# Kernel tuning notes

Measured on AMD Instinct MI355X. Metric: run time of the kernel, lower is better.

## Reference

```python
import jax, jax.numpy as jnp
import numpy as np
from jax import lax

T = 16          # timesteps
EPS = 1e-12     # torch F.normalize eps
DN = ('NCHW', 'OIHW', 'NCHW')

def conv2d(x, w, pad):
    return lax.conv_general_dilated(x, w, (1, 1), [(pad, pad), (pad, pad)],
                                    dimension_numbers=DN)

def setup_inputs() -> dict:
    key = jax.random.key(0)
    ks = jax.random.split(key, 7)
    B, C, H, W, K = 16, 512, 14, 14, 64
    return {
        'input_tensor': jax.random.normal(ks[0], (B * T, C, H, W), jnp.float32),
        'centers': jax.random.normal(ks[1], (K, C), jnp.float32) * 0.05,
        'share_w': jax.random.normal(ks[2], (K, C, 1, 1), jnp.float32) * 0.05,
        'share_b': jax.random.uniform(ks[3], (K,), jnp.float32),
        'U_z': jax.random.normal(ks[4], (K, K, 3, 3), jnp.float32) * 0.05,
        'U_r': jax.random.normal(ks[5], (K, K, 3, 3), jnp.float32) * 0.05,
        'U_h': jax.random.normal(ks[6], (K, K, 3, 3), jnp.float32) * 0.05,
    }

def reference(input_tensor, centers, share_w, share_b, U_z, U_r, U_h):
    NT, C, H, W = input_tensor.shape
    B = NT // T
    K = centers.shape[0]

    # soft-assignment pre-activation: 1x1 conv (SAME) -> [B*T, K, H, W]
    wxb = conv2d(input_tensor, share_w, 0) + share_b[None, :, None, None]
    wxb = wxb.reshape(B, T, K, H, W).transpose(1, 0, 2, 3, 4)  # [T,B,K,H,W]

    def gru_step(h, wxb_t):
        z = jax.nn.sigmoid(wxb_t + conv2d(h, U_z, 1))
        r = jax.nn.sigmoid(wxb_t + conv2d(h, U_r, 1))
        hh = jnp.tanh(wxb_t + conv2d(r * h, U_h, 1))
        h_new = (1.0 - z) * hh + z * h
        return h_new, h_new

    h0 = jnp.zeros((B, K, H, W), input_tensor.dtype)
    _, assign = lax.scan(gru_step, h0, wxb)            # [T,B,K,H,W]
    assign = assign.transpose(1, 0, 2, 3, 4).reshape(B * T, K, H * W)

    a_sum = assign.sum(-1, keepdims=True)              # [BT,K,1]
    a = a_sum * centers[None]                          # [BT,K,C]
    feats = input_tensor.reshape(B * T, C, H * W)
    x = jnp.einsum('nks,ncs->nkc', assign, feats)      # [BT,K,C]

    vlad = (x - a).reshape(B, T, K, C).sum(1)          # [B,K,C]
    vlad = vlad / jnp.maximum(jnp.linalg.norm(vlad, axis=2, keepdims=True), EPS)
    vlad = vlad.reshape(B, K * C)
    vlad = vlad / jnp.maximum(jnp.linalg.norm(vlad, axis=1, keepdims=True), EPS)
    return vlad
```

## Files before the change

kernel.cpp:

```cpp
#include <hip/hip_runtime.h>

#define Bc 16
#define Tc 16
#define Cc 512
#define Kc 64
#define Sc 196
#define KS (Kc*Sc)
#define BKS (Bc*Kc*Sc)
#define TBKS (Tc*BKS)
#define GFIN (16*64*512)
#define PART_N (8*GFIN)
#define PX 256
#define PLB2 (Kc*PX)
#define NUTT 110592

typedef __attribute__((ext_vector_type(8))) short bf16x8;
typedef __attribute__((ext_vector_type(4))) float f32x4;

__device__ __forceinline__ float sigmoid_f(float x) { return 1.f / (1.f + __expf(-x)); }
__device__ __forceinline__ float tanh_f(float x) { return 1.f - 2.f / (__expf(2.f * x) + 1.f); }

__device__ __forceinline__ float b2f(unsigned short u) {
    return __uint_as_float(((unsigned)u) << 16);
}
__device__ __forceinline__ unsigned short f2b(float f) {
    unsigned u = __float_as_uint(f);
    return (unsigned short)((u + 0x7FFFu + ((u >> 16) & 1u)) >> 16);
}
__device__ __forceinline__ void split1(float f, unsigned short& h, unsigned short& l) {
    unsigned u = __float_as_uint(f);
    unsigned uh = u & 0xffff0000u;
    h = (unsigned short)(uh >> 16);
    float fl = f - __uint_as_float(uh);
    l = (unsigned short)(__float_as_uint(fl) >> 16);
}

__global__ __launch_bounds__(256) void k_transpose_w(const float* __restrict__ w, float* __restrict__ wt) {
    int idx = blockIdx.x * 256 + threadIdx.x;
    if (idx < Kc * Cc) {
        int k = idx & 63, c = idx >> 6;
        wt[idx] = w[k * Cc + c];
    }
}

__global__ __launch_bounds__(256) void k_prep_u(const float* __restrict__ Uz,
        const float* __restrict__ Ur, const float* __restrict__ Uh,
        unsigned short* __restrict__ uth, unsigned short* __restrict__ utl) {
    int idx = blockIdx.x * 256 + threadIdx.x;
    int ki = idx & 63;
    int ko = (idx >> 6) & 63;
    int gt = idx >> 12;
    int tap = gt % 9, g = gt / 9;
    const float* U = (g == 0) ? Uz : (g == 1) ? Ur : Uh;
    float v = U[((size_t)ko * 64 + ki) * 9 + tap];
    unsigned short h, l;
    split1(v, h, l);
    uth[idx] = h; utl[idx] = l;
}

__global__ __launch_bounds__(256) void k_init(float4* __restrict__ h32,
        float4* __restrict__ h16, float4* __restrict__ rh16) {
    const int i = blockIdx.x * 256 + threadIdx.x;
    const float4 z = make_float4(0.f, 0.f, 0.f, 0.f);
    h32[i] = z;
    if (i < 32768) { h16[i] = z; rh16[i] = z; }
}

__global__ __launch_bounds__(256) void k_conv1x1(const float* __restrict__ x, const float* __restrict__ wt,
        const float* __restrict__ bias, float* __restrict__ wxb,
        float* __restrict__ assign0, float* __restrict__ hplane32,
        unsigned short* __restrict__ hplane16) {
    __shared__ float Xs[64][64];
    const int tid = threadIdx.x;
    const int gs0 = blockIdx.x * 64;
    const int kw = __builtin_amdgcn_readfirstlane((tid >> 6) << 4);
    const int lane = tid & 63;
    const int rbase = (tid >> 6) * 16;
    const int gs_c = gs0 + lane;
    const int n_c = gs_c / Sc, s_c = gs_c - n_c * Sc;
    const float* xcol = x + (size_t)n_c * (Cc * Sc) + s_c;

    float xr[16];
#pragma unroll
    for (int q = 0; q < 16; ++q) xr[q] = xcol[(size_t)(rbase + q) * Sc];
    float acc[16] = {};
    for (int c0 = 0; c0 < Cc; c0 += 64) {
        __syncthreads();
#pragma unroll
        for (int q = 0; q < 16; ++q) Xs[rbase + q][lane] = xr[q];
        __syncthreads();
        if (c0 + 64 < Cc) {
#pragma unroll
            for (int q = 0; q < 16; ++q) xr[q] = xcol[(size_t)(c0 + 64 + rbase + q) * Sc];
        }
#pragma unroll 8
        for (int cc = 0; cc < 64; ++cc) {
            const float xv = Xs[cc][lane];
            const float* wp = wt + (size_t)(c0 + cc) * Kc + kw;
#pragma unroll
            for (int i = 0; i < 16; ++i) acc[i] += wp[i] * xv;
        }
    }
    const int t = n_c & 15, bb = n_c >> 4;
    float* op = wxb + (((size_t)t * Bc + bb) * Kc + kw) * Sc + s_c;
    const int px0 = (s_c / 14 + 1) * 16 + (s_c - (s_c / 14) * 14 + 1);
#pragma unroll
    for (int i = 0; i < 16; ++i) {
        float v = acc[i] + bias[kw + i];
        op[(size_t)i * Sc] = v;
        if (t == 0) {
            float a = (1.f - sigmoid_f(v)) * tanh_f(v);
            assign0[((size_t)bb * Kc + kw + i) * Sc + s_c] = a;
            const size_t pp = (size_t)bb * PLB2 + (size_t)px0 * 64 + kw + i;
            hplane32[pp] = a; hplane16[pp] = f2b(a);
        }
    }
}

__global__ __launch_bounds__(128) void k_gru_gates(const unsigned short* __restrict__ hplane16,
        const float* __restrict__ wxb_t, const unsigned short* __restrict__ uth,
        const unsigned short* __restrict__ utl,
        float* __restrict__ zb, unsigned short* __restrict__ rhplane16) {
    const int b = blockIdx.x, yrow = blockIdx.y + 1, gate = blockIdx.z;
    const int pxb = yrow * 16;
    const int tid = threadIdx.x;
    const int nh = tid >> 6;
    const int lane = tid & 63;
    const int lg = lane >> 4, ln = lane & 15;
    const unsigned short* hp = hplane16 + (size_t)b * PLB2;
    const unsigned short* ug_h = uth + (size_t)gate * 36864;
    const unsigned short* ug_l = utl + (size_t)gate * 36864;

    f32x4 acc[2];
    acc[0] = (f32x4){0.f, 0.f, 0.f, 0.f};
    acc[1] = (f32x4){0.f, 0.f, 0.f, 0.f};
#pragma unroll
    for (int tap = 0; tap < 9; ++tap) {
        const int toff = (tap / 3 - 1) * 16 + (tap % 3 - 1);
        int arow = pxb + ln + toff;
        arow = min(max(arow, 0), 255);
        const unsigned short* abase = hp + (size_t)arow * 64;
#pragma unroll
        for (int ks = 0; ks < 2; ++ks) {
            bf16x8 A = *(const bf16x8*)(abase + ks * 32 + lg * 8);
#pragma unroll
            for (int nt = 0; nt < 2; ++nt) {
                const int ko_t = (nh * 2 + nt) * 16;
                const size_t bo = ((size_t)tap * 64 + ko_t + ln) * 64 + ks * 32 + lg * 8;
                bf16x8 Bh = *(const bf16x8*)(ug_h + bo);
                bf16x8 Bl = *(const bf16x8*)(ug_l + bo);
                acc[nt] = __builtin_amdgcn_mfma_f32_16x16x32_bf16(A, Bh, acc[nt], 0, 0, 0);
                acc[nt] = __builtin_amdgcn_mfma_f32_16x16x32_bf16(A, Bl, acc[nt], 0, 0, 0);
            }
        }
    }
#pragma unroll
    for (int nt = 0; nt < 2; ++nt) {
        const int ko = (nh * 2 + nt) * 16 + ln;
#pragma unroll
        for (int r = 0; r < 4; ++r) {
            const int i = lg * 4 + r;
            if (i >= 1 && i <= 14) {
                const int s = (yrow - 1) * 14 + (i - 1);
                const size_t cs = ((size_t)b * Kc + ko) * Sc + s;
                float sv = sigmoid_f(wxb_t[cs] + acc[nt][r]);
                if (gate == 0) {
                    zb[cs] = sv;
                } else {
                    const int px = pxb + i;
                    float hv = b2f(hp[(size_t)px * 64 + ko]);
                    rhplane16[(size_t)b * PLB2 + (size_t)px * 64 + ko] = f2b(sv * hv);
                }
            }
        }
    }
}

__global__ __launch_bounds__(256) void k_gru_out(const unsigned short* __restrict__ rhplane16,
        const float* __restrict__ wxb_t, const unsigned short* __restrict__ uth,
        const unsigned short* __restrict__ utl, const float* __restrict__ zb,
        float* __restrict__ hplane32, unsigned short* __restrict__ hplane16,
        float* __restrict__ assign_t) {
    const int b = blockIdx.x, yrow = blockIdx.y + 1;
    const int pxb = yrow * 16;
    const int tid = threadIdx.x;
    const int nt = tid >> 6;
    const int lane = tid & 63;
    const int lg = lane >> 4, ln = lane & 15;
    const unsigned short* rp = rhplane16 + (size_t)b * PLB2;
    const unsigned short* uh0 = uth + (size_t)2 * 36864;
    const unsigned short* ul0 = utl + (size_t)2 * 36864;

    f32x4 acc = (f32x4){0.f, 0.f, 0.f, 0.f};
#pragma unroll
    for (int tap = 0; tap < 9; ++tap) {
        const int toff = (tap / 3 - 1) * 16 + (tap % 3 - 1);
        int arow = pxb + ln + toff;
        arow = min(max(arow, 0), 255);
        const unsigned short* abase = rp + (size_t)arow * 64;
#pragma unroll
        for (int ks = 0; ks < 2; ++ks) {
            bf16x8 A = *(const bf16x8*)(abase + ks * 32 + lg * 8);
            const size_t bo = ((size_t)tap * 64 + nt * 16 + ln) * 64 + ks * 32 + lg * 8;
            bf16x8 Bh = *(const bf16x8*)(uh0 + bo);
            bf16x8 Bl = *(const bf16x8*)(ul0 + bo);
            acc = __builtin_amdgcn_mfma_f32_16x16x32_bf16(A, Bh, acc, 0, 0, 0);
            acc = __builtin_amdgcn_mfma_f32_16x16x32_bf16(A, Bl, acc, 0, 0, 0);
        }
    }
    const int ko = nt * 16 + ln;
#pragma unroll
    for (int r = 0; r < 4; ++r) {
        const int i = lg * 4 + r;
        if (i >= 1 && i <= 14) {
            const int s = (yrow - 1) * 14 + (i - 1);
            const size_t cs = ((size_t)b * Kc + ko) * Sc + s;
            const int px = pxb + i;
            const size_t pp = (size_t)b * PLB2 + (size_t)px * 64 + ko;
            float pre = wxb_t[cs];
            float zv = zb[cs];
            float hpv = hplane32[pp];
            float hh = tanh_f(pre + acc[r]);
            float hn = (1.f - zv) * hh + zv * hpv;
            hplane32[pp] = hn;
            hplane16[pp] = f2b(hn);
            assign_t[cs] = hn;
        }
    }
}

__global__ __launch_bounds__(512) void k_einsum(const float* __restrict__ x, const float* __restrict__ assign,
                                                float* __restrict__ part) {
    extern __shared__ float lds[];
    unsigned short* Ah = (unsigned short*)lds;
    unsigned short* Al = Ah + 64 * 40;
    unsigned short* Xh = Al + 64 * 40;
    unsigned short* Xl = Xh + 128 * 40;
    const int cq = blockIdx.x, tg = blockIdx.y, b = blockIdx.z;
    const int tid = threadIdx.x;
    const int wv = tid >> 6, lane = tid & 63;
    const int lg = lane >> 4, ln = lane & 15;
    const int ka = tid >> 3, ss4 = (tid & 7) * 4;
    const int cx = tid >> 2, ss8 = (tid & 3) * 8;

    f32x4 acc[4];
#pragma unroll
    for (int mt = 0; mt < 4; ++mt) acc[mt] = (f32x4){0.f, 0.f, 0.f, 0.f};

    for (int tt = 0; tt < 2; ++tt) {
        const int t = tg * 2 + tt;
        const int n = b * Tc + t;
        const float* ap = assign + ((size_t)t * Bc + b) * KS;
        const float* xp = x + ((size_t)n * Cc + cq * 128) * Sc;
        for (int sc7 = 0; sc7 < 7; ++sc7) {
            const int s0 = sc7 * 32;
            __syncthreads();
            {
                float4 v = make_float4(0.f, 0.f, 0.f, 0.f);
                if (s0 + ss4 <= 192) v = *(const float4*)(ap + (size_t)ka * Sc + s0 + ss4);
                ushort4 h, l;
                split1(v.x, h.x, l.x); split1(v.y, h.y, l.y);
                split1(v.z, h.z, l.z); split1(v.w, h.w, l.w);
                *(ushort4*)(Ah + ka * 40 + ss4) = h;
                *(ushort4*)(Al + ka * 40 + ss4) = l;
            }
#pragma unroll
            for (int q = 0; q < 2; ++q) {
                const int so = ss8 + q * 4;
                float4 v = make_float4(0.f, 0.f, 0.f, 0.f);
                if (s0 + so <= 192) v = *(const float4*)(xp + (size_t)cx * Sc + s0 + so);
                ushort4 h, l;
                split1(v.x, h.x, l.x); split1(v.y, h.y, l.y);
                split1(v.z, h.z, l.z); split1(v.w, h.w, l.w);
                *(ushort4*)(Xh + cx * 40 + so) = h;
                *(ushort4*)(Xl + cx * 40 + so) = l;
            }
            __syncthreads();
            bf16x8 Bh = *(const bf16x8*)(Xh + (wv * 16 + ln) * 40 + lg * 8);
            bf16x8 Bl = *(const bf16x8*)(Xl + (wv * 16 + ln) * 40 + lg * 8);
#pragma unroll
            for (int mt = 0; mt < 4; ++mt) {
                bf16x8 Af = *(const bf16x8*)(Ah + (mt * 16 + ln) * 40 + lg * 8);
                bf16x8 Alo = *(const bf16x8*)(Al + (mt * 16 + ln) * 40 + lg * 8);
                acc[mt] = __builtin_amdgcn_mfma_f32_16x16x32_bf16(Af, Bh, acc[mt], 0, 0, 0);
                acc[mt] = __builtin_amdgcn_mfma_f32_16x16x32_bf16(Alo, Bh, acc[mt], 0, 0, 0);
                acc[mt] = __builtin_amdgcn_mfma_f32_16x16x32_bf16(Af, Bl, acc[mt], 0, 0, 0);
            }
        }
    }
    const int c = cq * 128 + wv * 16 + ln;
#pragma unroll
    for (int mt = 0; mt < 4; ++mt) {
#pragma unroll
        for (int r = 0; r < 4; ++r) {
            const int k = mt * 16 + lg * 4 + r;
            part[(((size_t)tg * Bc + b) * Kc + k) * Cc + c] = acc[mt][r];
        }
    }
}

__global__ __launch_bounds__(256) void k_reduce(const float* __restrict__ assign, const float* __restrict__ part,
        const float* __restrict__ centers, float* __restrict__ vlad, float* __restrict__ norm2) {
    __shared__ float redw[4];
    __shared__ float a_s;
    const int blk = blockIdx.x;
    const int b = blk >> 6, k = blk & 63;
    const int tid = threadIdx.x;
    const int wave = tid >> 6, lane = tid & 63;
    const size_t bkoff = ((size_t)b * Kc + k) * Sc;
    float s = 0.f;
    for (int q = tid; q < 784; q += 256) {
        int t = q / 49, s4 = q - t * 49;
        float4 v = *(const float4*)(assign + (size_t)t * BKS + bkoff + s4 * 4);
        s += (v.x + v.y) + (v.z + v.w);
    }
#pragma unroll
    for (int o = 1; o < 64; o <<= 1) s += __shfl_xor(s, o);
    if (lane == 0) redw[wave] = s;
    __syncthreads();
    if (tid == 0) a_s = redw[0] + redw[1] + redw[2] + redw[3];
    __syncthreads();
    const float a = a_s;
    const size_t base = ((size_t)b * Kc + k) * Cc;
    const int c = tid * 2;
    float2 acc2 = make_float2(0.f, 0.f);
#pragma unroll
    for (int g = 0; g < 8; ++g) {
        float2 p = *(const float2*)(part + (size_t)g * GFIN + base + c);
        acc2.x += p.x; acc2.y += p.y;
    }
    float2 cv = *(const float2*)(centers + (size_t)k * Cc + c);
    float v0 = acc2.x - a * cv.x, v1 = acc2.y - a * cv.y;
    *(float2*)(vlad + base + c) = make_float2(v0, v1);
    float ss = v0 * v0 + v1 * v1;
#pragma unroll
    for (int o = 1; o < 64; o <<= 1) ss += __shfl_xor(ss, o);
    __syncthreads();
    if (lane == 0) redw[wave] = ss;
    __syncthreads();
    if (tid == 0) norm2[blk] = redw[0] + redw[1] + redw[2] + redw[3];
}

__global__ __launch_bounds__(64) void k_norms(const float* __restrict__ norm2, float* __restrict__ scl) {
    const int b = blockIdx.x;
    const int k = threadIdx.x;
    float ss = norm2[b * Kc + k];
    float inv = 1.f / fmaxf(sqrtf(ss), 1e-12f);
    float g = ss * inv * inv;
#pragma unroll
    for (int o = 1; o < 64; o <<= 1) g += __shfl_xor(g, o);
    float gi = 1.f / fmaxf(sqrtf(g), 1e-12f);
    scl[b * Kc + k] = inv * gi;
}

__global__ __launch_bounds__(256) void k_scale(const float* __restrict__ vlad, const float* __restrict__ scl,
                                               float* __restrict__ out) {
    const int blk = blockIdx.x;
    const int b = blk >> 4, kt = blk & 15;
    const int tid = threadIdx.x;
    const int kk = tid >> 6, lane = tid & 63;
    const int k = kt * 4 + kk;
    const float sv = scl[b * Kc + k];
    const float* vp = vlad + ((size_t)b * Kc + k) * Cc + lane * 8;
    float* op = out + ((size_t)b * Kc + k) * Cc + lane * 8;
    float4 v0 = *(const float4*)vp;
    float4 v1 = *(const float4*)(vp + 4);
    *(float4*)op = make_float4(v0.x * sv, v0.y * sv, v0.z * sv, v0.w * sv);
    *(float4*)(op + 4) = make_float4(v1.x * sv, v1.y * sv, v1.z * sv, v1.w * sv);
}

extern "C" void kernel_launch(void* const* d_in, const int* in_sizes, int n_in,
                              void* d_out, int out_size, void* d_ws, size_t ws_size,
                              hipStream_t stream) {
    (void)in_sizes; (void)n_in; (void)out_size; (void)ws_size;
    const float* x       = (const float*)d_in[0];
    const float* centers = (const float*)d_in[1];
    const float* share_w = (const float*)d_in[2];
    const float* share_b = (const float*)d_in[3];
    const float* Uz      = (const float*)d_in[4];
    const float* Ur      = (const float*)d_in[5];
    const float* Uh      = (const float*)d_in[6];
    float* out = (float*)d_out;
    float* ws  = (float*)d_ws;

    float* part      = ws;
    float* vlad      = ws;
    float* wxb       = ws;
    unsigned short* rhplane16 = (unsigned short*)(ws + (size_t)TBKS);
    unsigned short* hplane16  = (unsigned short*)(ws + (size_t)TBKS + 131072);
    float* assign   = ws + (size_t)PART_N;
    float* zb       = assign + (size_t)TBKS;
    float* hplane32 = zb + (size_t)BKS;
    float* wt       = hplane32 + (size_t)Bc * PLB2;
    unsigned short* utt_h = (unsigned short*)(wt + 32768);
    unsigned short* utt_l = utt_h + NUTT;
    float* norm2    = wt + 32768 + NUTT;
    float* scl      = norm2 + (size_t)Bc * Kc;

    const size_t ein_lds = (64 * 40 + 128 * 40) * 2 * 2;

    k_transpose_w<<<dim3(128), 256, 0, stream>>>(share_w, wt);
    k_prep_u<<<dim3(432), 256, 0, stream>>>(Uz, Ur, Uh, utt_h, utt_l);
    k_init<<<dim3(256), 256, 0, stream>>>((float4*)hplane32, (float4*)hplane16, (float4*)rhplane16);
    k_conv1x1<<<dim3(784), 256, 0, stream>>>(x, wt, share_b, wxb, assign, hplane32, hplane16);
    for (int t = 1; t < Tc; ++t) {
        k_gru_gates<<<dim3(16, 14, 2), 128, 0, stream>>>(hplane16, wxb + (size_t)t * BKS,
                                                         utt_h, utt_l, zb, rhplane16);
        k_gru_out<<<dim3(16, 14), 256, 0, stream>>>(rhplane16, wxb + (size_t)t * BKS,
                                                    utt_h, utt_l, zb, hplane32, hplane16,
                                                    assign + (size_t)t * BKS);
    }
    k_einsum<<<dim3(4, 8, 16), 512, ein_lds, stream>>>(x, assign, part);
    k_reduce<<<dim3(Bc * Kc), 256, 0, stream>>>(assign, part, centers, vlad, norm2);
    k_norms<<<dim3(Bc), 64, 0, stream>>>(norm2, scl);
    k_scale<<<dim3(256), 256, 0, stream>>>(vlad, scl, out);
}
```

Measured before the change: 455.7 us.

## Fuse GRU gate and output kernels into one step kernel with LDS r*h halo

Merges the two per-timestep GRU kernels into a single kernel. Three waves recompute the r gate for the centre row and its neighbour rows into a swizzled LDS tile, one wave computes z into LDS, and two waves then run the U_h convolution from LDS. The bf16 hidden plane is double-buffered across timesteps to avoid read/write races, which halves the launch count in the 15-step loop and removes the global round trips for z and r*h. In exchange, the r gate is computed redundantly for halo rows, and only two of the four waves run the final convolution.

```diff
diff --git a/kernel.cpp b/kernel.cpp
--- a/kernel.cpp
+++ b/kernel.cpp
@@ -58,12 +58,11 @@
     uth[idx] = h; utl[idx] = l;
 }
 
-__global__ __launch_bounds__(256) void k_init(float4* __restrict__ h32,
-        float4* __restrict__ h16, float4* __restrict__ rh16) {
+__global__ __launch_bounds__(256) void k_init(float4* __restrict__ h32, float4* __restrict__ h16) {
     const int i = blockIdx.x * 256 + threadIdx.x;
     const float4 z = make_float4(0.f, 0.f, 0.f, 0.f);
     h32[i] = z;
-    if (i < 32768) { h16[i] = z; rh16[i] = z; }
+    h16[i] = z;
 }
 
 __global__ __launch_bounds__(256) void k_conv1x1(const float* __restrict__ x, const float* __restrict__ wt,
@@ -117,114 +116,116 @@
     }
 }
 
-__global__ __launch_bounds__(128) void k_gru_gates(const unsigned short* __restrict__ hplane16,
-        const float* __restrict__ wxb_t, const unsigned short* __restrict__ uth,
-        const unsigned short* __restrict__ utl,
-        float* __restrict__ zb, unsigned short* __restrict__ rhplane16) {
-    const int b = blockIdx.x, yrow = blockIdx.y + 1, gate = blockIdx.z;
-    const int pxb = yrow * 16;
+__global__ __launch_bounds__(256) void k_gru_step(const unsigned short* __restrict__ h16r,
+        unsigned short* __restrict__ h16w, float* __restrict__ hplane32,
+        const float* __restrict__ wxb_t,
+        const unsigned short* __restrict__ uth, const unsigned short* __restrict__ utl,
+        float* __restrict__ assign_t) {
+    __shared__ unsigned short rhS[48 * 64];
+    __shared__ float zS[16 * 68];
+    const int b = blockIdx.x, y0 = blockIdx.y + 1;
     const int tid = threadIdx.x;
-    const int nh = tid >> 6;
-    const int lane = tid & 63;
+    const int w = tid >> 6, lane = tid & 63;
     const int lg = lane >> 4, ln = lane & 15;
-    const unsigned short* hp = hplane16 + (size_t)b * PLB2;
-    const unsigned short* ug_h = uth + (size_t)gate * 36864;
-    const unsigned short* ug_l = utl + (size_t)gate * 36864;
-
-    f32x4 acc[2];
-    acc[0] = (f32x4){0.f, 0.f, 0.f, 0.f};
-    acc[1] = (f32x4){0.f, 0.f, 0.f, 0.f};
-#pragma unroll
-    for (int tap = 0; tap < 9; ++tap) {
-        const int toff = (tap / 3 - 1) * 16 + (tap % 3 - 1);
-        int arow = pxb + ln + toff;
-        arow = min(max(arow, 0), 255);
-        const unsigned short* abase = hp + (size_t)arow * 64;
-#pragma unroll
-        for (int ks = 0; ks < 2; ++ks) {
-            bf16x8 A = *(const bf16x8*)(abase + ks * 32 + lg * 8);
-#pragma unroll
-            for (int nt = 0; nt < 2; ++nt) {
-                const int ko_t = (nh * 2 + nt) * 16;
-                const size_t bo = ((size_t)tap * 64 + ko_t + ln) * 64 + ks * 32 + lg * 8;
-                bf16x8 Bh = *(const bf16x8*)(ug_h + bo);
-                bf16x8 Bl = *(const bf16x8*)(ug_l + bo);
-                acc[nt] = __builtin_amdgcn_mfma_f32_16x16x32_bf16(A, Bh, acc[nt], 0, 0, 0);
-                acc[nt] = __builtin_amdgcn_mfma_f32_16x16x32_bf16(A, Bl, acc[nt], 0, 0, 0);
-            }
-        }
-    }
-#pragma unroll
-    for (int nt = 0; nt < 2; ++nt) {
-        const int ko = (nh * 2 + nt) * 16 + ln;
-#pragma unroll
-        for (int r = 0; r < 4; ++r) {
-            const int i = lg * 4 + r;
-            if (i >= 1 && i <= 14) {
-                const int s = (yrow - 1) * 14 + (i - 1);
-                const size_t cs = ((size_t)b * Kc + ko) * Sc + s;
-                float sv = sigmoid_f(wxb_t[cs] + acc[nt][r]);
-                if (gate == 0) {
-                    zb[cs] = sv;
+    const unsigned short* hp = h16r + (size_t)b * PLB2;
+
+    {
+        const int prow = (w < 3) ? (y0 - 1 + w) : y0;
+        const int gsel = (w < 3) ? 1 : 0;
+        const unsigned short* gh = uth + (size_t)gsel * 36864;
+        const unsigned short* gl = utl + (size_t)gsel * 36864;
+        f32x4 acc[4];
+#pragma unroll
+        for (int nt = 0; nt < 4; ++nt) acc[nt] = (f32x4){0.f, 0.f, 0.f, 0.f};
+#pragma unroll
+        for (int tap = 0; tap < 9; ++tap) {
+            const int toff = (tap / 3 - 1) * 16 + (tap % 3 - 1);
+            int arow = prow * 16 + ln + toff;
+            arow = min(max(arow, 0), 255);
+            const unsigned short* ab = hp + (size_t)arow * 64;
+#pragma unroll
+            for (int ks = 0; ks < 2; ++ks) {
+                bf16x8 A = *(const bf16x8*)(ab + ks * 32 + lg * 8);
+#pragma unroll
+                for (int nt = 0; nt < 4; ++nt) {
+                    const size_t bo = ((size_t)tap * 64 + nt * 16 + ln) * 64 + ks * 32 + lg * 8;
+                    bf16x8 Bh = *(const bf16x8*)(gh + bo);
+                    bf16x8 Bl = *(const bf16x8*)(gl + bo);
+                    acc[nt] = __builtin_amdgcn_mfma_f32_16x16x32_bf16(A, Bh, acc[nt], 0, 0, 0);
+                    acc[nt] = __builtin_amdgcn_mfma_f32_16x16x32_bf16(A, Bl, acc[nt], 0, 0, 0);
+                }
+            }
+        }
+        const int srow = prow - 1;
+#pragma unroll
+        for (int nt = 0; nt < 4; ++nt) {
+#pragma unroll
+            for (int r = 0; r < 4; ++r) {
+                const int i = lg * 4 + r;
+                const int ko = nt * 16 + ln;
+                const bool sval = (srow >= 0 && srow < 14 && i >= 1 && i <= 14);
+                const int s = sval ? srow * 14 + (i - 1) : 0;
+                const float pre = wxb_t[((size_t)b * Kc + ko) * Sc + s];
+                const float g = sigmoid_f(pre + acc[nt][r]);
+                if (w < 3) {
+                    const int px = prow * 16 + i;
+                    const float hv = b2f(hp[(size_t)px * 64 + ko]);
+                    const int lpx = w * 16 + i;
+                    *(unsigned short*)((char*)rhS + lpx * 128 + ((ko << 1) ^ ((lpx & 7) << 4))) = f2b(g * hv);
                 } else {
-                    const int px = pxb + i;
-                    float hv = b2f(hp[(size_t)px * 64 + ko]);
-                    rhplane16[(size_t)b * PLB2 + (size_t)px * 64 + ko] = f2b(sv * hv);
+                    zS[i * 68 + ko] = g;
                 }
             }
         }
     }
-}
-
-__global__ __launch_bounds__(256) void k_gru_out(const unsigned short* __restrict__ rhplane16,
-        const float* __restrict__ wxb_t, const unsigned short* __restrict__ uth,
-        const unsigned short* __restrict__ utl, const float* __restrict__ zb,
-        float* __restrict__ hplane32, unsigned short* __restrict__ hplane16,
-        float* __restrict__ assign_t) {
-    const int b = blockIdx.x, yrow = blockIdx.y + 1;
-    const int pxb = yrow * 16;
-    const int tid = threadIdx.x;
-    const int nt = tid >> 6;
-    const int lane = tid & 63;
-    const int lg = lane >> 4, ln = lane & 15;
-    const unsigned short* rp = rhplane16 + (size_t)b * PLB2;
-    const unsigned short* uh0 = uth + (size_t)2 * 36864;
-    const unsigned short* ul0 = utl + (size_t)2 * 36864;
-
-    f32x4 acc = (f32x4){0.f, 0.f, 0.f, 0.f};
-#pragma unroll
-    for (int tap = 0; tap < 9; ++tap) {
-        const int toff = (tap / 3 - 1) * 16 + (tap % 3 - 1);
-        int arow = pxb + ln + toff;
-        arow = min(max(arow, 0), 255);
-        const unsigned short* abase = rp + (size_t)arow * 64;
-#pragma unroll
-        for (int ks = 0; ks < 2; ++ks) {
-            bf16x8 A = *(const bf16x8*)(abase + ks * 32 + lg * 8);
-            const size_t bo = ((size_t)tap * 64 + nt * 16 + ln) * 64 + ks * 32 + lg * 8;
-            bf16x8 Bh = *(const bf16x8*)(uh0 + bo);
-            bf16x8 Bl = *(const bf16x8*)(ul0 + bo);
-            acc = __builtin_amdgcn_mfma_f32_16x16x32_bf16(A, Bh, acc, 0, 0, 0);
-            acc = __builtin_amdgcn_mfma_f32_16x16x32_bf16(A, Bl, acc, 0, 0, 0);
-        }
-    }
-    const int ko = nt * 16 + ln;
-#pragma unroll
-    for (int r = 0; r < 4; ++r) {
-        const int i = lg * 4 + r;
-        if (i >= 1 && i <= 14) {
-            const int s = (yrow - 1) * 14 + (i - 1);
-            const size_t cs = ((size_t)b * Kc + ko) * Sc + s;
-            const int px = pxb + i;
-            const size_t pp = (size_t)b * PLB2 + (size_t)px * 64 + ko;
-            float pre = wxb_t[cs];
-            float zv = zb[cs];
-            float hpv = hplane32[pp];
-            float hh = tanh_f(pre + acc[r]);
-            float hn = (1.f - zv) * hh + zv * hpv;
-            hplane32[pp] = hn;
-            hplane16[pp] = f2b(hn);
-            assign_t[cs] = hn;
+    __syncthreads();
+    if (w < 2) {
+        const unsigned short* hh_t = uth + (size_t)2 * 36864;
+        const unsigned short* hl_t = utl + (size_t)2 * 36864;
+        f32x4 a2[2];
+        a2[0] = (f32x4){0.f, 0.f, 0.f, 0.f};
+        a2[1] = (f32x4){0.f, 0.f, 0.f, 0.f};
+#pragma unroll
+        for (int tap = 0; tap < 9; ++tap) {
+            const int toff = (tap / 3 - 1) * 16 + (tap % 3 - 1);
+            int la = 16 + ln + toff;
+            la = min(max(la, 0), 47);
+#pragma unroll
+            for (int ks = 0; ks < 2; ++ks) {
+                bf16x8 A = *(const bf16x8*)((const char*)rhS + la * 128 +
+                                            (((ks * 64 + lg * 16)) ^ ((la & 7) << 4)));
+#pragma unroll
+                for (int nt2 = 0; nt2 < 2; ++nt2) {
+                    const int kot = (w * 2 + nt2) * 16;
+                    const size_t bo = ((size_t)tap * 64 + kot + ln) * 64 + ks * 32 + lg * 8;
+                    bf16x8 Bh = *(const bf16x8*)(hh_t + bo);
+                    bf16x8 Bl = *(const bf16x8*)(hl_t + bo);
+                    a2[nt2] = __builtin_amdgcn_mfma_f32_16x16x32_bf16(A, Bh, a2[nt2], 0, 0, 0);
+                    a2[nt2] = __builtin_amdgcn_mfma_f32_16x16x32_bf16(A, Bl, a2[nt2], 0, 0, 0);
+                }
+            }
+        }
+#pragma unroll
+        for (int nt2 = 0; nt2 < 2; ++nt2) {
+#pragma unroll
+            for (int r = 0; r < 4; ++r) {
+                const int i = lg * 4 + r;
+                if (i >= 1 && i <= 14) {
+                    const int ko = (w * 2 + nt2) * 16 + ln;
+                    const int s = (y0 - 1) * 14 + (i - 1);
+                    const size_t cs = ((size_t)b * Kc + ko) * Sc + s;
+                    const int px = y0 * 16 + i;
+                    const size_t pp = (size_t)b * PLB2 + (size_t)px * 64 + ko;
+                    const float pre = wxb_t[cs];
+                    const float zv = zS[i * 68 + ko];
+                    const float hpv = hplane32[pp];
+                    const float hh = tanh_f(pre + a2[nt2][r]);
+                    const float hn = (1.f - zv) * hh + zv * hpv;
+                    hplane32[pp] = hn;
+                    h16w[pp] = f2b(hn);
+                    assign_t[cs] = hn;
+                }
+            }
         }
     }
 }
@@ -386,11 +387,10 @@
     float* part      = ws;
     float* vlad      = ws;
     float* wxb       = ws;
-    unsigned short* rhplane16 = (unsigned short*)(ws + (size_t)TBKS);
-    unsigned short* hplane16  = (unsigned short*)(ws + (size_t)TBKS + 131072);
+    unsigned short* h16A = (unsigned short*)(ws + (size_t)TBKS);
+    unsigned short* h16B = h16A + (size_t)Bc * PLB2;
     float* assign   = ws + (size_t)PART_N;
-    float* zb       = assign + (size_t)TBKS;
-    float* hplane32 = zb + (size_t)BKS;
+    float* hplane32 = assign + (size_t)TBKS;
     float* wt       = hplane32 + (size_t)Bc * PLB2;
     unsigned short* utt_h = (unsigned short*)(wt + 32768);
     unsigned short* utt_l = utt_h + NUTT;
@@ -401,14 +401,15 @@
 
     k_transpose_w<<<dim3(128), 256, 0, stream>>>(share_w, wt);
     k_prep_u<<<dim3(432), 256, 0, stream>>>(Uz, Ur, Uh, utt_h, utt_l);
-    k_init<<<dim3(256), 256, 0, stream>>>((float4*)hplane32, (float4*)hplane16, (float4*)rhplane16);
-    k_conv1x1<<<dim3(784), 256, 0, stream>>>(x, wt, share_b, wxb, assign, hplane32, hplane16);
+    k_init<<<dim3(256), 256, 0, stream>>>((float4*)hplane32, (float4*)h16A);
+    k_conv1x1<<<dim3(784), 256, 0, stream>>>(x, wt, share_b, wxb, assign, hplane32, h16A);
     for (int t = 1; t < Tc; ++t) {
-        k_gru_gates<<<dim3(16, 14, 2), 128, 0, stream>>>(hplane16, wxb + (size_t)t * BKS,
-                                                         utt_h, utt_l, zb, rhplane16);
-        k_gru_out<<<dim3(16, 14), 256, 0, stream>>>(rhplane16, wxb + (size_t)t * BKS,
-                                                    utt_h, utt_l, zb, hplane32, hplane16,
-                                                    assign + (size_t)t * BKS);
+        const unsigned short* rbuf = (t & 1) ? h16A : h16B;
+        unsigned short* wbuf = (t & 1) ? h16B : h16A;
+        k_gru_step<<<dim3(16, 14), 256, 0, stream>>>(rbuf, wbuf, hplane32,
+                                                     wxb + (size_t)t * BKS,
+                                                     utt_h, utt_l,
+                                                     assign + (size_t)t * BKS);
     }
     k_einsum<<<dim3(4, 8, 16), 512, ein_lds, stream>>>(x, assign, part);
     k_reduce<<<dim3(Bc * Kc), 256, 0, stream>>>(assign, part, centers, vlad, norm2);
```

Result: slower. 580.5 us (+27.4%).
